# Optimization experiments

Measured on AMD Instinct MI355X. Metric: run time of the kernel, lower is better.

The kernel has to match this reference:

```python
import jax, jax.numpy as jnp
import numpy as np

N_EDGES = 1_000_000
N_PARTICLES = 50_000
NUM_RADIAL = 16
EMBED = 128
OUT_EMBED = 256
NUM_TARGETS = 1


def setup_inputs() -> dict:
    key = jax.random.key(0)
    ks = jax.random.split(key, 12)
    s = lambda fan_in: 1.0 / np.sqrt(fan_in)
    inp = {
        'messages': jax.random.normal(ks[0], (N_EDGES, EMBED), jnp.float32),
        'rbf': jax.random.normal(ks[1], (N_EDGES, NUM_RADIAL), jnp.float32),
        'idx_i': jax.random.randint(ks[2], (N_EDGES,), 0, N_PARTICLES),
        'idx_j': jax.random.randint(ks[3], (N_EDGES,), 0, N_PARTICLES),
        'W_rbf': jax.random.normal(ks[4], (NUM_RADIAL, EMBED), jnp.float32) * s(NUM_RADIAL),
        'W_up': jax.random.normal(ks[5], (EMBED, OUT_EMBED), jnp.float32) * s(EMBED),
        'W1': jax.random.normal(ks[6], (OUT_EMBED, OUT_EMBED), jnp.float32) * s(OUT_EMBED),
        'b1': jnp.zeros((OUT_EMBED,), jnp.float32),
        'W2': jax.random.normal(ks[7], (OUT_EMBED, OUT_EMBED), jnp.float32) * s(OUT_EMBED),
        'b2': jnp.zeros((OUT_EMBED,), jnp.float32),
        'W3': jax.random.normal(ks[8], (OUT_EMBED, OUT_EMBED), jnp.float32) * s(OUT_EMBED),
        'b3': jnp.zeros((OUT_EMBED,), jnp.float32),
        'W_final': jax.random.normal(ks[9], (OUT_EMBED, NUM_TARGETS), jnp.float32) * s(OUT_EMBED),
    }
    return inp


def reference(messages, rbf, idx_i, idx_j, W_rbf, W_up, W1, b1, W2, b2, W3, b3, W_final):
    # RBF gate: [E, NUM_RADIAL] @ [NUM_RADIAL, EMBED] -> [E, EMBED]
    transformed_rbf = rbf @ W_rbf
    gated = messages * transformed_rbf  # elementwise, [E, EMBED]
    # scatter-add per receiving atom idx_i -> [N_PARTICLES, EMBED]
    summed = jax.ops.segment_sum(gated, idx_i, num_segments=N_PARTICLES)
    h = summed @ W_up
    h = jax.nn.swish(h @ W1 + b1)
    h = jax.nn.swish(h @ W2 + b2)
    h = jax.nn.swish(h @ W3 + b3)
    per_atom_targets = h @ W_final  # [N_PARTICLES, NUM_TARGETS]
    return per_atom_targets
```

## Files before the change

### kernel.cpp

```cpp
#include <hip/hip_runtime.h>
#include <hip/hip_bf16.h>

#define EMBED 128
#define NRAD  16
#define OUTE  256

typedef __bf16 bf16x8 __attribute__((ext_vector_type(8)));
typedef float  f32x4  __attribute__((ext_vector_type(4)));

static __device__ __forceinline__ unsigned short f2bf(float x) {
    return __builtin_bit_cast(unsigned short, (__bf16)x);
}

#define RLF(X, L) __builtin_bit_cast(float, \
    __builtin_amdgcn_readlane(__builtin_bit_cast(int, (X)), (L)))

__global__ __launch_bounds__(256) void zero_fill_kernel(uint4* __restrict__ dst, int n4)
{
    const uint4 z = {0u, 0u, 0u, 0u};
    for (int i = blockIdx.x * blockDim.x + threadIdx.x; i < n4;
         i += gridDim.x * blockDim.x)
        dst[i] = z;
}

__global__ __launch_bounds__(256) void hist_kernel(const int* __restrict__ idx_i,
                                                   int* __restrict__ counts, int n_edges)
{
    for (int e = blockIdx.x * blockDim.x + threadIdx.x; e < n_edges;
         e += gridDim.x * blockDim.x)
        atomicAdd(&counts[idx_i[e]], 1);
}

__global__ __launch_bounds__(1024) void scan_kernel(const int* __restrict__ counts,
                                                    int* __restrict__ cursor, int n)
{
    __shared__ int partial[1024];
    const int tid = threadIdx.x;
    const int chunk = (n + 1023) / 1024;
    const int lo = min(tid * chunk, n), hi = min(lo + chunk, n);
    int s = 0;
    for (int i = lo; i < hi; ++i) s += counts[i];
    partial[tid] = s;
    __syncthreads();
    for (int off = 1; off < 1024; off <<= 1) {
        int v = (tid >= off) ? partial[tid - off] : 0;
        __syncthreads();
        partial[tid] += v;
        __syncthreads();
    }
    int run = (tid > 0) ? partial[tid - 1] : 0;
    for (int i = lo; i < hi; ++i) {
        cursor[i] = run;
        run += counts[i];
    }
}

__global__ __launch_bounds__(256) void scatter_ids_kernel(const int* __restrict__ idx_i,
                                                          int* __restrict__ cursor,
                                                          int2* __restrict__ eid_pid,
                                                          int n_edges)
{
    for (int e = blockIdx.x * blockDim.x + threadIdx.x; e < n_edges;
         e += gridDim.x * blockDim.x) {
        const int i = idx_i[e];
        const int pos = atomicAdd(&cursor[i], 1);
        eid_pid[pos] = make_int2(e, i);
    }
}

#define SEGSTEP(P, M, T)                                                    \
    do {                                                                    \
        if ((P) != cur) {                                                   \
            if (first) {                                                    \
                atomicAdd(&summed[(long long)cur * EMBED + col], ax);       \
                atomicAdd(&summed[(long long)cur * EMBED + col + 1], ay);   \
                first = false;                                              \
            } else {                                                        \
                *reinterpret_cast<float2*>(                                 \
                    &summed[(long long)cur * EMBED + col]) =                \
                    make_float2(ax, ay);                                    \
            }                                                               \
            ax = 0.f; ay = 0.f; cur = (P);                                  \
        }                                                                   \
        ax = fmaf((M).x, (T).x, ax);                                        \
        ay = fmaf((M).y, (T).y, ay);                                        \
    } while (0)

#define MSG_ISSUE(S, QPOS)                                                  \
    {                                                                       \
        const int eT0 = __shfl(myE, (QPOS) + 0, 64);                        \
        const int eT1 = __shfl(myE, (QPOS) + 1, 64);                        \
        const int eT2 = __shfl(myE, (QPOS) + 2, 64);                        \
        const int eT3 = __shfl(myE, (QPOS) + 3, 64);                        \
        S##0 = *reinterpret_cast<const float2*>(                            \
            messages + (long long)eT0 * EMBED + col);                       \
        S##1 = *reinterpret_cast<const float2*>(                            \
            messages + (long long)eT1 * EMBED + col);                       \
        S##2 = *reinterpret_cast<const float2*>(                            \
            messages + (long long)eT2 * EMBED + col);                       \
        S##3 = *reinterpret_cast<const float2*>(                            \
            messages + (long long)eT3 * EMBED + col);                       \
    }

#define DOT_EDGE(TX, TY, L)                                                      \
    {                                                                            \
        float v_;                                                                \
        TX = 0.f; TY = 0.f;                                                      \
        v_ = RLF(ra.x, L); TX = fmaf(v_, w[0].x, TX);  TY = fmaf(v_, w[0].y, TY);  \
        v_ = RLF(ra.y, L); TX = fmaf(v_, w[1].x, TX);  TY = fmaf(v_, w[1].y, TY);  \
        v_ = RLF(ra.z, L); TX = fmaf(v_, w[2].x, TX);  TY = fmaf(v_, w[2].y, TY);  \
        v_ = RLF(ra.w, L); TX = fmaf(v_, w[3].x, TX);  TY = fmaf(v_, w[3].y, TY);  \
        v_ = RLF(rb.x, L); TX = fmaf(v_, w[4].x, TX);  TY = fmaf(v_, w[4].y, TY);  \
        v_ = RLF(rb.y, L); TX = fmaf(v_, w[5].x, TX);  TY = fmaf(v_, w[5].y, TY);  \
        v_ = RLF(rb.z, L); TX = fmaf(v_, w[6].x, TX);  TY = fmaf(v_, w[6].y, TY);  \
        v_ = RLF(rb.w, L); TX = fmaf(v_, w[7].x, TX);  TY = fmaf(v_, w[7].y, TY);  \
        v_ = RLF(rc.x, L); TX = fmaf(v_, w[8].x, TX);  TY = fmaf(v_, w[8].y, TY);  \
        v_ = RLF(rc.y, L); TX = fmaf(v_, w[9].x, TX);  TY = fmaf(v_, w[9].y, TY);  \
        v_ = RLF(rc.z, L); TX = fmaf(v_, w[10].x, TX); TY = fmaf(v_, w[10].y, TY); \
        v_ = RLF(rc.w, L); TX = fmaf(v_, w[11].x, TX); TY = fmaf(v_, w[11].y, TY); \
        v_ = RLF(rd.x, L); TX = fmaf(v_, w[12].x, TX); TY = fmaf(v_, w[12].y, TY); \
        v_ = RLF(rd.y, L); TX = fmaf(v_, w[13].x, TX); TY = fmaf(v_, w[13].y, TY); \
        v_ = RLF(rd.z, L); TX = fmaf(v_, w[14].x, TX); TY = fmaf(v_, w[14].y, TY); \
        v_ = RLF(rd.w, L); TX = fmaf(v_, w[15].x, TX); TY = fmaf(v_, w[15].y, TY); \
    }

__global__ __launch_bounds__(256, 4) void gated_segsum_kernel(
    const float* __restrict__ messages, const float* __restrict__ rbf,
    const int2* __restrict__ eid_pid,
    const float* __restrict__ W_rbf, float* __restrict__ summed, int n_edges)
{
    const int lane = threadIdx.x & 63;
    const int wv   = threadIdx.x >> 6;
    const int col  = lane * 2;

    float2 w[NRAD];
#pragma unroll
    for (int r = 0; r < NRAD; ++r)
        w[r] = *reinterpret_cast<const float2*>(&W_rbf[r * EMBED + col]);

    const int nwin = (n_edges + 63) >> 6;
    for (int win = blockIdx.x * 4 + wv; win < nwin; win += gridDim.x * 4) {
        const int w0 = win << 6;
        const int nq = min(n_edges - w0, 64);

        float ax = 0.f, ay = 0.f;
        bool first = true;

        if (nq == 64) {
            const int2 ep = eid_pid[w0 + lane];
            const int myE = ep.x;
            const int myP = ep.y;
            int cur = __builtin_amdgcn_readlane(myP, 0);

            const float4* R = reinterpret_cast<const float4*>(rbf + (long long)myE * NRAD);
            const float4 ra = R[0], rb = R[1], rc = R[2], rd = R[3];

            float2 cA0, cA1, cA2, cA3, cB0, cB1, cB2, cB3, cC0, cC1, cC2, cC3;
            MSG_ISSUE(cA, 0)
            MSG_ISSUE(cB, 4)

            for (int q = 0; q < 16; ++q) {
                if (q < 14) { MSG_ISSUE(cC, (q + 2) * 4) }

                const int base = q * 4;
                float t0x, t0y, t1x, t1y, t2x, t2y, t3x, t3y;
                DOT_EDGE(t0x, t0y, base + 0)
                DOT_EDGE(t1x, t1y, base + 1)
                DOT_EDGE(t2x, t2y, base + 2)
                DOT_EDGE(t3x, t3y, base + 3)
                const int p0 = __builtin_amdgcn_readlane(myP, base + 0);
                const int p1 = __builtin_amdgcn_readlane(myP, base + 1);
                const int p2 = __builtin_amdgcn_readlane(myP, base + 2);
                const int p3 = __builtin_amdgcn_readlane(myP, base + 3);
                const float2 t0 = make_float2(t0x, t0y);
                const float2 t1 = make_float2(t1x, t1y);
                const float2 t2 = make_float2(t2x, t2y);
                const float2 t3 = make_float2(t3x, t3y);

                SEGSTEP(p0, cA0, t0);
                SEGSTEP(p1, cA1, t1);
                SEGSTEP(p2, cA2, t2);
                SEGSTEP(p3, cA3, t3);

                cA0 = cB0; cA1 = cB1; cA2 = cB2; cA3 = cB3;
                cB0 = cC0; cB1 = cC1; cB2 = cC2; cB3 = cC3;
            }
            atomicAdd(&summed[(long long)cur * EMBED + col], ax);
            atomicAdd(&summed[(long long)cur * EMBED + col + 1], ay);
        } else {
            int cur = eid_pid[w0].y;
            for (int q = 0; q < nq; ++q) {
                const int2 ep = eid_pid[w0 + q];
                const float2 m = *reinterpret_cast<const float2*>(
                    messages + (long long)ep.x * EMBED + col);
                const float4* R =
                    reinterpret_cast<const float4*>(rbf + (long long)ep.x * NRAD);
                const float4 q0 = R[0], q1 = R[1], q2 = R[2], q3 = R[3];
                const float rv[NRAD] = {q0.x, q0.y, q0.z, q0.w, q1.x, q1.y, q1.z, q1.w,
                                        q2.x, q2.y, q2.z, q2.w, q3.x, q3.y, q3.z, q3.w};
                float tx = 0.f, ty = 0.f;
#pragma unroll
                for (int r = 0; r < NRAD; ++r) {
                    tx = fmaf(rv[r], w[r].x, tx);
                    ty = fmaf(rv[r], w[r].y, ty);
                }
                const float2 t = make_float2(tx, ty);
                SEGSTEP(ep.y, m, t);
            }
            atomicAdd(&summed[(long long)cur * EMBED + col], ax);
            atomicAdd(&summed[(long long)cur * EMBED + col + 1], ay);
        }
    }
}

__global__ __launch_bounds__(256) void prep_weights_kernel(
    const float* __restrict__ Wup, const float* __restrict__ W1,
    const float* __restrict__ W2, const float* __restrict__ W3,
    __bf16* __restrict__ WupT, __bf16* __restrict__ W1T,
    __bf16* __restrict__ W2T, __bf16* __restrict__ W3T)
{
    const int total = OUTE * EMBED + 3 * OUTE * OUTE;
    for (int id = blockIdx.x * blockDim.x + threadIdx.x; id < total;
         id += gridDim.x * blockDim.x) {
        if (id < OUTE * EMBED) {
            const int n = id / EMBED, k = id % EMBED;
            WupT[id] = (__bf16)Wup[k * OUTE + n];
        } else {
            const int r = id - OUTE * EMBED;
            const int wsel = r / (OUTE * OUTE);
            const int rr = r % (OUTE * OUTE);
            const int n = rr / OUTE, k = rr % OUTE;
            const float* src = (wsel == 0) ? W1 : ((wsel == 1) ? W2 : W3);
            __bf16* dst = (wsel == 0) ? W1T : ((wsel == 1) ? W2T : W3T);
            dst[rr] = (__bf16)src[k * OUTE + n];
        }
    }
}

template <int K, bool ACT>
__device__ __forceinline__ void mlp_layer(const unsigned short* lin, unsigned short* lout,
                                          const __bf16* __restrict__ Wt,
                                          const float* __restrict__ bias, int l, int w)
{
    f32x4 acc[4][4];
#pragma unroll
    for (int i = 0; i < 4; ++i)
#pragma unroll
        for (int j = 0; j < 4; ++j)
            acc[i][j] = (f32x4){0.f, 0.f, 0.f, 0.f};

    const int lr = l & 15;
    const int hi = l >> 4;
    const int kg = hi * 8;

#pragma unroll
    for (int kk = 0; kk < K; kk += 32) {
        bf16x8 af[4], bf_[4];
#pragma unroll
        for (int i = 0; i < 4; ++i) {
            const int row = i * 16 + lr;
            const int byte = row * 512 + (((kk + kg) * 2) ^ ((row & 7) << 4));
            af[i] = *reinterpret_cast<const bf16x8*>(
                reinterpret_cast<const char*>(lin) + byte);
        }
#pragma unroll
        for (int j = 0; j < 4; ++j) {
            const int n = w * 64 + j * 16 + lr;
            bf_[j] = *reinterpret_cast<const bf16x8*>(Wt + (size_t)n * K + kk + kg);
        }
#pragma unroll
        for (int i = 0; i < 4; ++i)
#pragma unroll
            for (int j = 0; j < 4; ++j)
                acc[i][j] = __builtin_amdgcn_mfma_f32_16x16x32_bf16(af[i], bf_[j],
                                                                    acc[i][j], 0, 0, 0);
    }

    float bb[4];
#pragma unroll
    for (int j = 0; j < 4; ++j)
        bb[j] = ACT ? bias[w * 64 + j * 16 + lr] : 0.f;

#pragma unroll
    for (int j = 0; j < 4; ++j) {
        const int colb = (w * 64 + j * 16 + lr) * 2;
#pragma unroll
        for (int i = 0; i < 4; ++i) {
#pragma unroll
            for (int r = 0; r < 4; ++r) {
                const int row = i * 16 + hi * 4 + r;
                float v = acc[i][j][r];
                if (ACT) {
                    v += bb[j];
                    v = v / (1.f + __expf(-v));
                }
                const int byte = row * 512 + (colb ^ ((row & 7) << 4));
                *reinterpret_cast<unsigned short*>(
                    reinterpret_cast<char*>(lout) + byte) = f2bf(v);
            }
        }
    }
}

__global__ __launch_bounds__(256) void fused_mlp_kernel(
    const float* __restrict__ summed,
    const __bf16* __restrict__ WupT, const __bf16* __restrict__ W1T,
    const __bf16* __restrict__ W2T, const __bf16* __restrict__ W3T,
    const float* __restrict__ b1, const float* __restrict__ b2,
    const float* __restrict__ b3, const float* __restrict__ Wf,
    float* __restrict__ out, int M)
{
    __shared__ __align__(16) unsigned short buf0[64 * 256];
    __shared__ __align__(16) unsigned short buf1[64 * 256];

    const int tid = threadIdx.x;
    const int l = tid & 63, w = tid >> 6;
    const int row0 = blockIdx.x * 64;

#pragma unroll
    for (int i = 0; i < 8; ++i) {
        const int id = tid + i * 256;
        const int row = id >> 5;
        const int c = (id & 31) * 4;
        float4 v = make_float4(0.f, 0.f, 0.f, 0.f);
        const int gr = row0 + row;
        if (gr < M)
            v = *reinterpret_cast<const float4*>(summed + (long long)gr * EMBED + c);
        ushort4 u = make_ushort4(f2bf(v.x), f2bf(v.y), f2bf(v.z), f2bf(v.w));
        const int byte = row * 512 + ((c * 2) ^ ((row & 7) << 4));
        *reinterpret_cast<ushort4*>(reinterpret_cast<char*>(buf0) + byte) = u;
    }
    __syncthreads();

    mlp_layer<EMBED, false>(buf0, buf1, WupT, nullptr, l, w);
    __syncthreads();
    mlp_layer<OUTE, true>(buf1, buf0, W1T, b1, l, w);
    __syncthreads();
    mlp_layer<OUTE, true>(buf0, buf1, W2T, b2, l, w);
    __syncthreads();
    mlp_layer<OUTE, true>(buf1, buf0, W3T, b3, l, w);
    __syncthreads();

    const int row = tid >> 2, q = tid & 3;
    float s = 0.f;
#pragma unroll
    for (int c = 0; c < 8; ++c) {
        const int k = q * 64 + c * 8;
        const int byte = row * 512 + ((k * 2) ^ ((row & 7) << 4));
        const bf16x8 hv = *reinterpret_cast<const bf16x8*>(
            reinterpret_cast<const char*>(buf0) + byte);
        const float4 wa = *reinterpret_cast<const float4*>(Wf + k);
        const float4 wb = *reinterpret_cast<const float4*>(Wf + k + 4);
        s += (float)hv[0] * wa.x + (float)hv[1] * wa.y +
             (float)hv[2] * wa.z + (float)hv[3] * wa.w +
             (float)hv[4] * wb.x + (float)hv[5] * wb.y +
             (float)hv[6] * wb.z + (float)hv[7] * wb.w;
    }
    s += __shfl_xor(s, 1);
    s += __shfl_xor(s, 2);
    if (q == 0 && row0 + row < M) out[row0 + row] = s;
}

extern "C" void kernel_launch(void* const* d_in, const int* in_sizes, int n_in,
                              void* d_out, int out_size, void* d_ws, size_t ws_size,
                              hipStream_t stream)
{
    const float* messages = (const float*)d_in[0];
    const float* rbf      = (const float*)d_in[1];
    const int*   idx_i    = (const int*)d_in[2];
    const float* W_rbf    = (const float*)d_in[4];
    const float* W_up     = (const float*)d_in[5];
    const float* W1       = (const float*)d_in[6];
    const float* b1       = (const float*)d_in[7];
    const float* W2       = (const float*)d_in[8];
    const float* b2       = (const float*)d_in[9];
    const float* W3       = (const float*)d_in[10];
    const float* b3       = (const float*)d_in[11];
    const float* Wf       = (const float*)d_in[12];
    float* out = (float*)d_out;

    const int n_edges = in_sizes[2];
    const int M = out_size;

    char* ws = (char*)d_ws;
    size_t off = 0;
    float* summed = (float*)(ws + off); off += (size_t)M * EMBED * sizeof(float);
    int* counts     = (int*)(ws + off); off += (size_t)M * sizeof(int);
    int* cursor     = (int*)(ws + off); off += (size_t)M * sizeof(int);
    off = (off + 7) & ~(size_t)7;
    int2* eid_pid   = (int2*)(ws + off); off += (size_t)n_edges * sizeof(int2);
    off = (off + 255) & ~(size_t)255;
    __bf16* WupT = (__bf16*)(ws + off); off += (size_t)OUTE * EMBED * 2;
    __bf16* W1T  = (__bf16*)(ws + off); off += (size_t)OUTE * OUTE * 2;
    __bf16* W2T  = (__bf16*)(ws + off); off += (size_t)OUTE * OUTE * 2;
    __bf16* W3T  = (__bf16*)(ws + off); off += (size_t)OUTE * OUTE * 2;

    const int n4 = (int)(((size_t)M * EMBED + M) / 4);
    zero_fill_kernel<<<2048, 256, 0, stream>>>((uint4*)summed, n4);

    hist_kernel<<<4096, 256, 0, stream>>>(idx_i, counts, n_edges);
    scan_kernel<<<1, 1024, 0, stream>>>(counts, cursor, M);
    scatter_ids_kernel<<<4096, 256, 0, stream>>>(idx_i, cursor, eid_pid, n_edges);
    prep_weights_kernel<<<896, 256, 0, stream>>>(W_up, W1, W2, W3, WupT, W1T, W2T, W3T);
    gated_segsum_kernel<<<2048, 256, 0, stream>>>(messages, rbf, eid_pid,
                                                  W_rbf, summed, n_edges);
    fused_mlp_kernel<<<(M + 63) / 64, 256, 0, stream>>>(summed, WupT, W1T, W2T, W3T,
                                                        b1, b2, b3, Wf, out, M);
}
```

Baseline: 454.9 us.

## Prefetch next window's edge ids, rbf and messages across segsum window iterations

The gated segment-sum kernel now software-pipelines across the windows each wave processes. It loads the next window's edge/particle ids early, fetches that window's rbf rows mid-loop, and issues its first message loads in the last two iterations of the current window. This is meant to hide the load latency at each window boundary. The grid is halved to 1024 blocks so each wave handles more windows, which costs extra registers and reduces parallelism.

```diff
diff --git a/kernel.cpp b/kernel.cpp
--- a/kernel.cpp
+++ b/kernel.cpp
@@ -86,12 +86,12 @@
         ay = fmaf((M).y, (T).y, ay);                                        \
     } while (0)
 
-#define MSG_ISSUE(S, QPOS)                                                  \
+#define MSG_ISSUE_E(S, SRC, QPOS)                                           \
     {                                                                       \
-        const int eT0 = __shfl(myE, (QPOS) + 0, 64);                        \
-        const int eT1 = __shfl(myE, (QPOS) + 1, 64);                        \
-        const int eT2 = __shfl(myE, (QPOS) + 2, 64);                        \
-        const int eT3 = __shfl(myE, (QPOS) + 3, 64);                        \
+        const int eT0 = __shfl((SRC), (QPOS) + 0, 64);                      \
+        const int eT1 = __shfl((SRC), (QPOS) + 1, 64);                      \
+        const int eT2 = __shfl((SRC), (QPOS) + 2, 64);                      \
+        const int eT3 = __shfl((SRC), (QPOS) + 3, 64);                      \
         S##0 = *reinterpret_cast<const float2*>(                            \
             messages + (long long)eT0 * EMBED + col);                       \
         S##1 = *reinterpret_cast<const float2*>(                            \
@@ -138,29 +138,53 @@
     for (int r = 0; r < NRAD; ++r)
         w[r] = *reinterpret_cast<const float2*>(&W_rbf[r * EMBED + col]);
 
-    const int nwin = (n_edges + 63) >> 6;
-    for (int win = blockIdx.x * 4 + wv; win < nwin; win += gridDim.x * 4) {
+    const int nwin      = (n_edges + 63) >> 6;
+    const int nwin_full = n_edges >> 6;
+    const int wstep     = gridDim.x * 4;
+
+    int win = blockIdx.x * 4 + wv;
+
+    int2   ep = make_int2(0, 0);
+    float4 ra, rb, rc, rd;
+    float2 cA0, cA1, cA2, cA3, cB0, cB1, cB2, cB3, cC0, cC1, cC2, cC3;
+
+    if (win < nwin_full) {
+        ep = eid_pid[(win << 6) + lane];
+        const float4* R = reinterpret_cast<const float4*>(rbf + (long long)ep.x * NRAD);
+        ra = R[0]; rb = R[1]; rc = R[2]; rd = R[3];
+        MSG_ISSUE_E(cA, ep.x, 0)
+        MSG_ISSUE_E(cB, ep.x, 4)
+    }
+
+    for (; win < nwin; win += wstep) {
         const int w0 = win << 6;
-        const int nq = min(n_edges - w0, 64);
-
-        float ax = 0.f, ay = 0.f;
-        bool first = true;
-
-        if (nq == 64) {
-            const int2 ep = eid_pid[w0 + lane];
+
+        if (win < nwin_full) {
             const int myE = ep.x;
             const int myP = ep.y;
-            int cur = __builtin_amdgcn_readlane(myP, 0);
-
-            const float4* R = reinterpret_cast<const float4*>(rbf + (long long)myE * NRAD);
-            const float4 ra = R[0], rb = R[1], rc = R[2], rd = R[3];
-
-            float2 cA0, cA1, cA2, cA3, cB0, cB1, cB2, cB3, cC0, cC1, cC2, cC3;
-            MSG_ISSUE(cA, 0)
-            MSG_ISSUE(cB, 4)
+            int  cur   = __builtin_amdgcn_readlane(myP, 0);
+            float ax = 0.f, ay = 0.f;
+            bool first = true;
+
+            const int  winN     = win + wstep;
+            const bool nextFull = (winN < nwin_full);
+            int2 epN = make_int2(0, 0);
+            if (nextFull) epN = eid_pid[(winN << 6) + lane];
+            float4 raN, rbN, rcN, rdN;
 
             for (int q = 0; q < 16; ++q) {
-                if (q < 14) { MSG_ISSUE(cC, (q + 2) * 4) }
+                if (q == 4 && nextFull) {
+                    const float4* RN =
+                        reinterpret_cast<const float4*>(rbf + (long long)epN.x * NRAD);
+                    raN = RN[0]; rbN = RN[1]; rcN = RN[2]; rdN = RN[3];
+                }
+                if (q <= 13) {
+                    MSG_ISSUE_E(cC, myE, (q + 2) * 4)
+                } else if (q == 14) {
+                    if (nextFull) MSG_ISSUE_E(cC, epN.x, 0)
+                } else {
+                    if (nextFull) MSG_ISSUE_E(cC, epN.x, 4)
+                }
 
                 const int base = q * 4;
                 float t0x, t0y, t1x, t1y, t2x, t2y, t3x, t3y;
@@ -187,14 +211,19 @@
             }
             atomicAdd(&summed[(long long)cur * EMBED + col], ax);
             atomicAdd(&summed[(long long)cur * EMBED + col + 1], ay);
+
+            if (nextFull) { ep = epN; ra = raN; rb = rbN; rc = rcN; rd = rdN; }
         } else {
+            const int nq = n_edges - w0;
+            float ax = 0.f, ay = 0.f;
+            bool first = true;
             int cur = eid_pid[w0].y;
             for (int q = 0; q < nq; ++q) {
-                const int2 ep = eid_pid[w0 + q];
+                const int2 epq = eid_pid[w0 + q];
                 const float2 m = *reinterpret_cast<const float2*>(
-                    messages + (long long)ep.x * EMBED + col);
+                    messages + (long long)epq.x * EMBED + col);
                 const float4* R =
-                    reinterpret_cast<const float4*>(rbf + (long long)ep.x * NRAD);
+                    reinterpret_cast<const float4*>(rbf + (long long)epq.x * NRAD);
                 const float4 q0 = R[0], q1 = R[1], q2 = R[2], q3 = R[3];
                 const float rv[NRAD] = {q0.x, q0.y, q0.z, q0.w, q1.x, q1.y, q1.z, q1.w,
                                         q2.x, q2.y, q2.z, q2.w, q3.x, q3.y, q3.z, q3.w};
@@ -205,7 +234,7 @@
                     ty = fmaf(rv[r], w[r].y, ty);
                 }
                 const float2 t = make_float2(tx, ty);
-                SEGSTEP(ep.y, m, t);
+                SEGSTEP(epq.y, m, t);
             }
             atomicAdd(&summed[(long long)cur * EMBED + col], ax);
             atomicAdd(&summed[(long long)cur * EMBED + col + 1], ay);
@@ -402,7 +431,7 @@
     scan_kernel<<<1, 1024, 0, stream>>>(counts, cursor, M);
     scatter_ids_kernel<<<4096, 256, 0, stream>>>(idx_i, cursor, eid_pid, n_edges);
     prep_weights_kernel<<<896, 256, 0, stream>>>(W_up, W1, W2, W3, WupT, W1T, W2T, W3T);
-    gated_segsum_kernel<<<2048, 256, 0, stream>>>(messages, rbf, eid_pid,
+    gated_segsum_kernel<<<1024, 256, 0, stream>>>(messages, rbf, eid_pid,
                                                   W_rbf, summed, n_edges);
     fused_mlp_kernel<<<(M + 63) / 64, 256, 0, stream>>>(summed, WupT, W1T, W2T, W3T,
                                                         b1, b2, b3, Wf, out, M);
```

Measured after the change: 456.4 us. About the same (+0.3%).
